# Optimization experiments

Measured on AMD Instinct MI355X. Metric: run time of the kernel, lower is better.

Reference implementation:

```python
import jax, jax.numpy as jnp
import numpy as np

D_MODEL = 1024
D_INNER = 2 * D_MODEL        # mambapy default expand=2
D_STATE = 16                 # mambapy default
D_CONV = 4                   # mambapy default
DT_RANK = D_MODEL // 16      # ceil(1024/16) = 64
D_FF = 4 * D_MODEL
BATCH = 2
SEQ = 2048


def setup_inputs() -> dict:
    key = jax.random.key(0)
    ks = jax.random.split(key, 12)
    s = 0.02
    rn = lambda k, shape: jax.random.normal(k, shape, jnp.float32) * s
    inp = {
        'x': jax.random.normal(ks[0], (BATCH, SEQ, D_MODEL), jnp.float32),
        'ln1_w': jnp.ones((D_MODEL,), jnp.float32),
        'ln1_b': jnp.zeros((D_MODEL,), jnp.float32),
        'in_proj_w': rn(ks[1], (2 * D_INNER, D_MODEL)),
        'conv_w': rn(ks[2], (D_INNER, 1, D_CONV)),
        'conv_b': jnp.zeros((D_INNER,), jnp.float32),
        'x_proj_w': rn(ks[3], (DT_RANK + 2 * D_STATE, D_INNER)),
        'dt_w': rn(ks[4], (D_INNER, DT_RANK)),
        'dt_b': jax.random.normal(ks[5], (D_INNER,), jnp.float32) * 0.5 - 4.0,
        'A_log': jnp.log(jnp.broadcast_to(jnp.arange(1, D_STATE + 1, dtype=jnp.float32), (D_INNER, D_STATE))),
        'Dskip': jnp.ones((D_INNER,), jnp.float32),
        'out_proj_w': rn(ks[6], (D_MODEL, D_INNER)),
        'ln2_w': jnp.ones((D_MODEL,), jnp.float32),
        'ln2_b': jnp.zeros((D_MODEL,), jnp.float32),
        'ff1_w': rn(ks[7], (D_FF, D_MODEL)),
        'ff1_b': jnp.zeros((D_FF,), jnp.float32),
        'ff2_w': rn(ks[8], (D_MODEL, D_FF)),
        'ff2_b': jnp.zeros((D_MODEL,), jnp.float32),
    }
    return inp


def _layernorm(x, w, b, eps=1e-5):
    m = jnp.mean(x, -1, keepdims=True)
    v = jnp.var(x, -1, keepdims=True)
    return (x - m) * jax.lax.rsqrt(v + eps) * w + b


def _mamba(y, in_proj_w, conv_w, conv_b, x_proj_w, dt_w, dt_b, A_log, Dskip, out_proj_w):
    # y: [B, L, d_model]
    xz = y @ in_proj_w.T                       # [B, L, 2*d_inner]
    xc, z = jnp.split(xz, 2, axis=-1)
    # causal depthwise conv1d over seq
    xt = xc.transpose(0, 2, 1)                 # [B, d_inner, L]
    xt = jax.lax.conv_general_dilated(
        xt, conv_w, (1,), [(D_CONV - 1, 0)],
        dimension_numbers=('NCH', 'OIH', 'NCH'),
        feature_group_count=D_INNER) + conv_b[None, :, None]
    u = jax.nn.silu(xt.transpose(0, 2, 1))     # [B, L, d_inner]
    dbc = u @ x_proj_w.T                       # [B, L, dt_rank + 2*d_state]
    dlt = jax.nn.softplus(dbc[..., :DT_RANK] @ dt_w.T + dt_b)   # [B, L, d_inner]
    Bm = dbc[..., DT_RANK:DT_RANK + D_STATE]   # [B, L, d_state]
    Cm = dbc[..., DT_RANK + D_STATE:]          # [B, L, d_state]
    A = -jnp.exp(A_log)                        # [d_inner, d_state]

    def step(h, inp):
        d, Bt, Ct, ut = inp                    # [B,d_inner],[B,d_state],[B,d_state],[B,d_inner]
        h = jnp.exp(d[:, :, None] * A) * h + (d * ut)[:, :, None] * Bt[:, None, :]
        yt = jnp.einsum('bds,bs->bd', h, Ct)
        return h, yt

    h0 = jnp.zeros((y.shape[0], D_INNER, D_STATE), y.dtype)
    xs = (dlt.transpose(1, 0, 2), Bm.transpose(1, 0, 2), Cm.transpose(1, 0, 2), u.transpose(1, 0, 2))
    _, ys = jax.lax.scan(step, h0, xs)         # ys: [L, B, d_inner]
    ysc = ys.transpose(1, 0, 2) + u * Dskip
    return (ysc * jax.nn.silu(z)) @ out_proj_w.T


def reference(x, ln1_w, ln1_b, in_proj_w, conv_w, conv_b, x_proj_w, dt_w, dt_b,
              A_log, Dskip, out_proj_w, ln2_w, ln2_b, ff1_w, ff1_b, ff2_w, ff2_b):
    y = _layernorm(x, ln1_w, ln1_b)
    y = _mamba(y, in_proj_w, conv_w, conv_b, x_proj_w, dt_w, dt_b, A_log, Dskip, out_proj_w)
    y = _layernorm(y, ln2_w, ln2_b)
    h = jax.nn.gelu(y @ ff1_w.T + ff1_b, approximate=False)
    y = h @ ff2_w.T + ff2_b
    return x + y
```

## Files before the change

kernel.cpp:

```cpp
#include <hip/hip_runtime.h>

#define DEV __device__ __forceinline__

typedef float f32x4 __attribute__((ext_vector_type(4)));
typedef short bf16x8 __attribute__((ext_vector_type(8)));

DEV unsigned short f2bf(float f) {
  union { float f; unsigned int u; } v; v.f = f;
  unsigned int r = v.u + 0x7FFFu + ((v.u >> 16) & 1u);
  return (unsigned short)(r >> 16);
}
DEV float bf2f(unsigned short h) {
  union { unsigned int u; float f; } v; v.u = ((unsigned int)h) << 16;
  return v.f;
}

DEV void gload16(const void* g, void* l) {
  __builtin_amdgcn_global_load_lds((const __attribute__((address_space(1))) void*)g,
                                   (__attribute__((address_space(3))) void*)l, 16, 0, 0);
}

template <int EPI>
__global__ __launch_bounds__(256) void gemm_bt(
    const unsigned short* __restrict__ A, const unsigned short* __restrict__ B,
    float* __restrict__ O1, float* __restrict__ O2, unsigned short* __restrict__ Ob,
    const float* __restrict__ bias, const float* __restrict__ resid,
    int M, int N, int K)
{
  __shared__ unsigned short As[128 * 64];
  __shared__ unsigned short Bs[128 * 64];
  const int tid = threadIdx.x;
  const int wave = tid >> 6;
  const int lane = tid & 63;
  const int brow = blockIdx.x * 128;
  const int bcol = blockIdx.y * 128;
  const int wr = (wave >> 1) * 64, wc = (wave & 1) * 64;
  const int lr = lane & 15, lq = lane >> 4;

  f32x4 acc[4][4];
#pragma unroll
  for (int m = 0; m < 4; ++m)
#pragma unroll
    for (int n = 0; n < 4; ++n)
#pragma unroll
      for (int j = 0; j < 4; ++j) acc[m][n][j] = 0.f;

  const size_t strideA = (size_t)K * 2;
  const char* Abase = (const char*)A + (size_t)brow * strideA;
  const char* Bbase = (const char*)B + (size_t)bcol * strideA;

  for (int k0 = 0; k0 < K; k0 += 64) {
#pragma unroll
    for (int is = 0; is < 4; ++is) {
      const int f = is * 4096 + tid * 16;
      const int row = f >> 7, colb = f & 127;
      char* la = (char*)As + is * 4096 + wave * 1024;
      char* lb = (char*)Bs + is * 4096 + wave * 1024;
      gload16(Abase + (size_t)row * strideA + (size_t)k0 * 2 + colb, la);
      gload16(Bbase + (size_t)row * strideA + (size_t)k0 * 2 + colb, lb);
    }
    asm volatile("s_waitcnt vmcnt(0)" ::: "memory");
    __syncthreads();
#pragma unroll
    for (int kk = 0; kk < 2; ++kk) {
      bf16x8 av[4], bv[4];
      const int ko = kk * 32 + lq * 8;
#pragma unroll
      for (int m = 0; m < 4; ++m)
        av[m] = *(const bf16x8*)&As[(wr + m * 16 + lr) * 64 + ko];
#pragma unroll
      for (int n = 0; n < 4; ++n)
        bv[n] = *(const bf16x8*)&Bs[(wc + n * 16 + lr) * 64 + ko];
#pragma unroll
      for (int m = 0; m < 4; ++m)
#pragma unroll
        for (int n = 0; n < 4; ++n)
          acc[m][n] = __builtin_amdgcn_mfma_f32_16x16x32_bf16(av[m], bv[n], acc[m][n], 0, 0, 0);
    }
    __syncthreads();
  }

#pragma unroll
  for (int m = 0; m < 4; ++m) {
#pragma unroll
    for (int n = 0; n < 4; ++n) {
      const int col = bcol + wc + n * 16 + lr;
      const int row0 = brow + wr + m * 16 + lq * 4;
#pragma unroll
      for (int j = 0; j < 4; ++j) {
        const int row = row0 + j;
        float v = acc[m][n][j];
        if (EPI == 0) {
          O1[(size_t)row * N + col] = v;
        } else if (EPI == 1) {
          v += bias[col];
          v = 0.5f * v * (1.f + erff(v * 0.70710678118654752f));
          Ob[(size_t)row * N + col] = f2bf(v);
        } else if (EPI == 2) {
          v += bias[col] + resid[(size_t)row * N + col];
          O1[(size_t)row * N + col] = v;
        } else if (EPI == 3) {
          v += bias[col];
          v = (v > 20.f) ? v : log1pf(expf(v));
          O1[(size_t)row * N + col] = v;
        } else {
          if (col < 2048) O1[(size_t)row * 2048 + col] = v;
          else O2[(size_t)row * 2048 + (col - 2048)] = v / (1.f + expf(-v));
        }
      }
    }
  }
}

__global__ __launch_bounds__(256) void ln_kernel(
    const float* __restrict__ x, const float* __restrict__ w,
    const float* __restrict__ b, unsigned short* __restrict__ out)
{
  const int row = blockIdx.x;
  const int tid = threadIdx.x;
  const float4 v = ((const float4*)(x + (size_t)row * 1024))[tid];
  float s = v.x + v.y + v.z + v.w;
  float sq = v.x * v.x + v.y * v.y + v.z * v.z + v.w * v.w;
#pragma unroll
  for (int m = 32; m >= 1; m >>= 1) { s += __shfl_xor(s, m); sq += __shfl_xor(sq, m); }
  __shared__ float ss[4], sqs[4];
  const int wave = tid >> 6;
  if ((tid & 63) == 0) { ss[wave] = s; sqs[wave] = sq; }
  __syncthreads();
  s = ss[0] + ss[1] + ss[2] + ss[3];
  sq = sqs[0] + sqs[1] + sqs[2] + sqs[3];
  const float mean = s * (1.f / 1024.f);
  const float var = sq * (1.f / 1024.f) - mean * mean;
  const float rstd = rsqrtf(var + 1e-5f);
  const float4 wv = ((const float4*)w)[tid];
  const float4 bv = ((const float4*)b)[tid];
  ushort4 o;
  o.x = f2bf((v.x - mean) * rstd * wv.x + bv.x);
  o.y = f2bf((v.y - mean) * rstd * wv.y + bv.y);
  o.z = f2bf((v.z - mean) * rstd * wv.z + bv.z);
  o.w = f2bf((v.w - mean) * rstd * wv.w + bv.w);
  ((ushort4*)(out + (size_t)row * 1024))[tid] = o;
}

__global__ __launch_bounds__(256) void conv_silu_kernel(
    const float* __restrict__ xc, const float* __restrict__ cw,
    const float* __restrict__ cb, unsigned short* __restrict__ u16)
{
  const int idx = blockIdx.x * 256 + threadIdx.x;
  const int d = idx & 2047;
  const int i = idx >> 11;
  const int t = i & 2047;
  float acc = cb[d];
#pragma unroll
  for (int k = 0; k < 4; ++k) {
    const int tt = t - 3 + k;
    if (tt >= 0) acc += xc[(size_t)(i - 3 + k) * 2048 + d] * cw[d * 4 + k];
  }
  const float s = acc / (1.f + expf(-acc));
  u16[idx] = f2bf(s);
}

__global__ void cvt_bf16_kernel(const float* __restrict__ s, unsigned short* __restrict__ d, int n4) {
  const int i = blockIdx.x * 256 + threadIdx.x;
  if (i >= n4) return;
  const float4 v = ((const float4*)s)[i];
  const ushort4 o = make_ushort4(f2bf(v.x), f2bf(v.y), f2bf(v.z), f2bf(v.w));
  ((ushort4*)d)[i] = o;
}

__global__ void cvt_xprojw_kernel(const float* __restrict__ s, unsigned short* __restrict__ d) {
  const int i = blockIdx.x * 256 + threadIdx.x;
  const int r = (i * 4) >> 11;
  ushort4 o;
  if (r < 96) {
    const float4 v = ((const float4*)s)[i];
    o = make_ushort4(f2bf(v.x), f2bf(v.y), f2bf(v.z), f2bf(v.w));
  } else {
    o = make_ushort4(0, 0, 0, 0);
  }
  ((ushort4*)d)[i] = o;
}

__global__ void cvt_adt_kernel(const float* __restrict__ dbc, unsigned short* __restrict__ adt) {
  const int idx = blockIdx.x * 256 + threadIdx.x;
  const int i = idx >> 6, r = idx & 63;
  adt[idx] = f2bf(dbc[(size_t)i * 128 + r]);
}

template <int NC>
__global__ __launch_bounds__(256) void scan_p1(
    const float* __restrict__ dlt, const unsigned short* __restrict__ u16,
    const float* __restrict__ dbc, const float* __restrict__ A_log,
    float* __restrict__ hpart, float* __restrict__ sdtp)
{
  constexpr int L = 2048 / NC;
  const int tid = threadIdx.x;
  const int c = blockIdx.x % NC;
  const int chg = blockIdx.x / NC;
  const int id = chg * 256 + tid;
  const int dch = id & 2047;
  const int b = id >> 11;
  float al2[16], h[16];
#pragma unroll
  for (int s = 0; s < 16; ++s) {
    al2[s] = -__expf(A_log[dch * 16 + s]) * 1.44269504f;
    h[s] = 0.f;
  }
  const int i0 = b * 2048 + c * L;
  float sdt = 0.f;
  for (int t = 0; t < L; ++t) {
    const size_t i = (size_t)(i0 + t);
    const float dt = dlt[i * 2048 + dch];
    const float uu = bf2f(u16[i * 2048 + dch]);
    const float dtu = dt * uu;
    const float* Bp = dbc + i * 128 + 64;
    const f32x4 B0 = *(const f32x4*)(Bp + 0);
    const f32x4 B1 = *(const f32x4*)(Bp + 4);
    const f32x4 B2 = *(const f32x4*)(Bp + 8);
    const f32x4 B3 = *(const f32x4*)(Bp + 12);
    sdt += dt;
#pragma unroll
    for (int s = 0; s < 16; ++s) {
      const float Bv = (s < 4) ? B0[s & 3] : (s < 8) ? B1[s & 3] : (s < 12) ? B2[s & 3] : B3[s & 3];
      h[s] = exp2f(dt * al2[s]) * h[s] + dtu * Bv;
    }
  }
  float* hp = hpart + ((size_t)(b * NC + c) * 2048 + dch) * 16;
#pragma unroll
  for (int s = 0; s < 16; ++s) hp[s] = h[s];
  sdtp[(size_t)(b * NC + c) * 2048 + dch] = sdt;
}

__global__ __launch_bounds__(256) void scan_prefix(
    const float* __restrict__ hpart, const float* __restrict__ sdtp,
    const float* __restrict__ A_log, float* __restrict__ hpre, int NC)
{
  const int g = blockIdx.x * 256 + threadIdx.x;
  const int s = g & 15;
  const int dch = (g >> 4) & 2047;
  const int b = g >> 15;
  const float al2 = -__expf(A_log[dch * 16 + s]) * 1.44269504f;
  float run = 0.f;
  for (int c = 0; c < NC; ++c) {
    const size_t base = ((size_t)(b * NC + c) * 2048 + dch) * 16 + s;
    hpre[base] = run;
    run = exp2f(al2 * sdtp[(size_t)(b * NC + c) * 2048 + dch]) * run + hpart[base];
  }
}

template <int NC>
__global__ __launch_bounds__(256) void scan_p2(
    const float* __restrict__ dlt, const unsigned short* u16,
    const float* __restrict__ dbc, const float* __restrict__ zs,
    const float* __restrict__ A_log, const float* __restrict__ Dskip,
    const float* __restrict__ hpre, unsigned short* gated)
{
  constexpr int L = 2048 / NC;
  const int tid = threadIdx.x;
  const int c = blockIdx.x % NC;
  const int chg = blockIdx.x / NC;
  const int id = chg * 256 + tid;
  const int dch = id & 2047;
  const int b = id >> 11;
  float al2[16], h[16];
#pragma unroll
  for (int s = 0; s < 16; ++s)
    al2[s] = -__expf(A_log[dch * 16 + s]) * 1.44269504f;
  const float* hb = hpre + ((size_t)(b * NC + c) * 2048 + dch) * 16;
#pragma unroll
  for (int s = 0; s < 16; ++s) h[s] = hb[s];
  const float Dsk = Dskip[dch];
  const int i0 = b * 2048 + c * L;
  for (int t = 0; t < L; ++t) {
    const size_t i = (size_t)(i0 + t);
    const float dt = dlt[i * 2048 + dch];
    const float uu = bf2f(u16[i * 2048 + dch]);
    const float zz = zs[i * 2048 + dch];
    const float dtu = dt * uu;
    const float* Bp = dbc + i * 128 + 64;
    const f32x4 B0 = *(const f32x4*)(Bp + 0);
    const f32x4 B1 = *(const f32x4*)(Bp + 4);
    const f32x4 B2 = *(const f32x4*)(Bp + 8);
    const f32x4 B3 = *(const f32x4*)(Bp + 12);
    const f32x4 C0 = *(const f32x4*)(Bp + 16);
    const f32x4 C1 = *(const f32x4*)(Bp + 20);
    const f32x4 C2 = *(const f32x4*)(Bp + 24);
    const f32x4 C3 = *(const f32x4*)(Bp + 28);
    float y0 = 0.f, y1 = 0.f, y2 = 0.f, y3 = 0.f;
#pragma unroll
    for (int s = 0; s < 16; ++s) {
      const float Bv = (s < 4) ? B0[s & 3] : (s < 8) ? B1[s & 3] : (s < 12) ? B2[s & 3] : B3[s & 3];
      const float Cv = (s < 4) ? C0[s & 3] : (s < 8) ? C1[s & 3] : (s < 12) ? C2[s & 3] : C3[s & 3];
      h[s] = exp2f(dt * al2[s]) * h[s] + dtu * Bv;
      if ((s & 3) == 0) y0 += h[s] * Cv;
      else if ((s & 3) == 1) y1 += h[s] * Cv;
      else if ((s & 3) == 2) y2 += h[s] * Cv;
      else y3 += h[s] * Cv;
    }
    const float y = (y0 + y1) + (y2 + y3);
    gated[i * 2048 + dch] = f2bf((y + uu * Dsk) * zz);
  }
}

extern "C" void kernel_launch(void* const* d_in, const int* in_sizes, int n_in,
                              void* d_out, int out_size, void* d_ws, size_t ws_size,
                              hipStream_t stream) {
  const float* x         = (const float*)d_in[0];
  const float* ln1_w     = (const float*)d_in[1];
  const float* ln1_b     = (const float*)d_in[2];
  const float* in_proj_w = (const float*)d_in[3];
  const float* conv_w    = (const float*)d_in[4];
  const float* conv_b    = (const float*)d_in[5];
  const float* x_proj_w  = (const float*)d_in[6];
  const float* dt_w      = (const float*)d_in[7];
  const float* dt_b      = (const float*)d_in[8];
  const float* A_log     = (const float*)d_in[9];
  const float* Dskip     = (const float*)d_in[10];
  const float* out_proj_w= (const float*)d_in[11];
  const float* ln2_w     = (const float*)d_in[12];
  const float* ln2_b     = (const float*)d_in[13];
  const float* ff1_w     = (const float*)d_in[14];
  const float* ff1_b     = (const float*)d_in[15];
  const float* ff2_w     = (const float*)d_in[16];
  const float* ff2_b     = (const float*)d_in[17];
  float* out = (float*)d_out;

  char* ws = (char*)d_ws;
  size_t off = 0;
  auto alloc = [&](size_t bytes) {
    char* p = ws + off;
    off += (bytes + 255) & ~(size_t)255;
    return p;
  };
  unsigned short* w16_in  = (unsigned short*)alloc(4096ull * 1024 * 2);
  unsigned short* w16_xp  = (unsigned short*)alloc(128ull * 2048 * 2);
  unsigned short* w16_dt  = (unsigned short*)alloc(2048ull * 64 * 2);
  unsigned short* w16_out = (unsigned short*)alloc(1024ull * 2048 * 2);
  unsigned short* w16_ff1 = (unsigned short*)alloc(4096ull * 1024 * 2);
  unsigned short* w16_ff2 = (unsigned short*)alloc(1024ull * 4096 * 2);
  unsigned short* y16     = (unsigned short*)alloc(4096ull * 1024 * 2);
  float* xcbuf            = (float*)alloc(4096ull * 2048 * 4);
  unsigned short* u16     = (unsigned short*)alloc(4096ull * 2048 * 2);
  float* slotA            = (float*)alloc(2048ull * 4096 * 4);
  float* zs               = (float*)alloc(2048ull * 4096 * 4);
  float* dbc              = (float*)alloc(4096ull * 128 * 4);
  unsigned short* adt16   = (unsigned short*)alloc(4096ull * 64 * 2);
  float* dlt              = (float*)alloc(2048ull * 4096 * 4);
  (void)ws_size; (void)in_sizes; (void)n_in; (void)out_size;

  constexpr int NC = 128;
  float* c2 = xcbuf;
  unsigned short* t2_16 = (unsigned short*)((char*)xcbuf + 4096ull * 1024 * 4);
  unsigned short* gated16 = u16;
  float* hpart = slotA;
  unsigned short* h16 = (unsigned short*)slotA;
  float* hpre  = xcbuf;
  float* sdtp  = (float*)y16;

  cvt_bf16_kernel<<<4096, 256, 0, stream>>>(in_proj_w, w16_in, 1048576);
  cvt_xprojw_kernel<<<256, 256, 0, stream>>>(x_proj_w, w16_xp);
  cvt_bf16_kernel<<<128, 256, 0, stream>>>(dt_w, w16_dt, 32768);
  cvt_bf16_kernel<<<2048, 256, 0, stream>>>(out_proj_w, w16_out, 524288);
  cvt_bf16_kernel<<<4096, 256, 0, stream>>>(ff1_w, w16_ff1, 1048576);
  cvt_bf16_kernel<<<4096, 256, 0, stream>>>(ff2_w, w16_ff2, 1048576);

  ln_kernel<<<4096, 256, 0, stream>>>(x, ln1_w, ln1_b, y16);
  gemm_bt<5><<<dim3(32, 32), 256, 0, stream>>>(y16, w16_in, xcbuf, zs, nullptr, nullptr, nullptr, 4096, 4096, 1024);
  conv_silu_kernel<<<32768, 256, 0, stream>>>(xcbuf, conv_w, conv_b, u16);
  gemm_bt<0><<<dim3(32, 1), 256, 0, stream>>>(u16, w16_xp, dbc, nullptr, nullptr, nullptr, nullptr, 4096, 128, 2048);
  cvt_adt_kernel<<<1024, 256, 0, stream>>>(dbc, adt16);
  gemm_bt<3><<<dim3(32, 16), 256, 0, stream>>>(adt16, w16_dt, dlt, nullptr, nullptr, dt_b, nullptr, 4096, 2048, 64);
  scan_p1<NC><<<16 * NC, 256, 0, stream>>>(dlt, u16, dbc, A_log, hpart, sdtp);
  scan_prefix<<<256, 256, 0, stream>>>(hpart, sdtp, A_log, hpre, NC);
  scan_p2<NC><<<16 * NC, 256, 0, stream>>>(dlt, u16, dbc, zs, A_log, Dskip, hpre, gated16);
  gemm_bt<0><<<dim3(32, 8), 256, 0, stream>>>(gated16, w16_out, c2, nullptr, nullptr, nullptr, nullptr, 4096, 1024, 2048);
  ln_kernel<<<4096, 256, 0, stream>>>(c2, ln2_w, ln2_b, t2_16);
  gemm_bt<1><<<dim3(32, 32), 256, 0, stream>>>(t2_16, w16_ff1, nullptr, nullptr, h16, ff1_b, nullptr, 4096, 4096, 1024);
  gemm_bt<2><<<dim3(32, 8), 256, 0, stream>>>(h16, w16_ff2, out, nullptr, nullptr, ff2_b, x, 4096, 1024, 4096);
}
```

Baseline: 720.4 us.

## Merge weight conversion launches, use hardware exp2, and stream pointers in scan

Six separate weight-conversion kernel launches become one combined kernel that dispatches on block index. The scan kernels now use the hardware v_exp_f32 instruction in place of library exp2f and __expf. Their per-step index arithmetic is replaced by incrementing pointers, with a wave-uniform base for the B/C loads, and restrict qualifiers are added. The gated output moves to a different buffer so it no longer aliases u16. The hardware exp trades some precision and denormal handling for fewer instructions in the scan's inner loop.

```diff
diff --git a/kernel.cpp b/kernel.cpp
--- a/kernel.cpp
+++ b/kernel.cpp
@@ -13,6 +13,18 @@
 DEV float bf2f(unsigned short h) {
   union { unsigned int u; float f; } v; v.u = ((unsigned int)h) << 16;
   return v.f;
+}
+
+DEV float fexp2(float x) {
+#if defined(__has_builtin)
+#if __has_builtin(__builtin_amdgcn_exp2f)
+  return __builtin_amdgcn_exp2f(x);
+#else
+  float r; asm("v_exp_f32 %0, %1" : "=v"(r) : "v"(x)); return r;
+#endif
+#else
+  float r; asm("v_exp_f32 %0, %1" : "=v"(r) : "v"(x)); return r;
+#endif
 }
 
 DEV void gload16(const void* g, void* l) {
@@ -160,25 +172,41 @@
   u16[idx] = f2bf(s);
 }
 
-__global__ void cvt_bf16_kernel(const float* __restrict__ s, unsigned short* __restrict__ d, int n4) {
-  const int i = blockIdx.x * 256 + threadIdx.x;
-  if (i >= n4) return;
-  const float4 v = ((const float4*)s)[i];
-  const ushort4 o = make_ushort4(f2bf(v.x), f2bf(v.y), f2bf(v.z), f2bf(v.w));
-  ((ushort4*)d)[i] = o;
-}
-
-__global__ void cvt_xprojw_kernel(const float* __restrict__ s, unsigned short* __restrict__ d) {
-  const int i = blockIdx.x * 256 + threadIdx.x;
-  const int r = (i * 4) >> 11;
-  ushort4 o;
-  if (r < 96) {
+__global__ __launch_bounds__(256) void cvt_weights(
+    const float* __restrict__ w_in, unsigned short* __restrict__ d_in16,
+    const float* __restrict__ w_ff1, unsigned short* __restrict__ d_ff1,
+    const float* __restrict__ w_ff2, unsigned short* __restrict__ d_ff2,
+    const float* __restrict__ w_out, unsigned short* __restrict__ d_out16,
+    const float* __restrict__ w_dt, unsigned short* __restrict__ d_dt,
+    const float* __restrict__ w_xp, unsigned short* __restrict__ d_xp)
+{
+  const int bid = blockIdx.x;
+  const int tid = threadIdx.x;
+  if (bid < 14336) {
+    const float* s; unsigned short* d; int lb;
+    if (bid < 4096)       { s = w_in;  d = d_in16;  lb = bid; }
+    else if (bid < 8192)  { s = w_ff1; d = d_ff1;   lb = bid - 4096; }
+    else if (bid < 12288) { s = w_ff2; d = d_ff2;   lb = bid - 8192; }
+    else if (bid < 14336) { s = w_out; d = d_out16; lb = bid - 12288; }
+    const int i = lb * 256 + tid;
     const float4 v = ((const float4*)s)[i];
-    o = make_ushort4(f2bf(v.x), f2bf(v.y), f2bf(v.z), f2bf(v.w));
+    ((ushort4*)d)[i] = make_ushort4(f2bf(v.x), f2bf(v.y), f2bf(v.z), f2bf(v.w));
+  } else if (bid < 14464) {
+    const int i = (bid - 14336) * 256 + tid;
+    const float4 v = ((const float4*)w_dt)[i];
+    ((ushort4*)d_dt)[i] = make_ushort4(f2bf(v.x), f2bf(v.y), f2bf(v.z), f2bf(v.w));
   } else {
-    o = make_ushort4(0, 0, 0, 0);
-  }
-  ((ushort4*)d)[i] = o;
+    const int i = (bid - 14464) * 256 + tid;
+    const int r = (i * 4) >> 11;
+    ushort4 o;
+    if (r < 96) {
+      const float4 v = ((const float4*)w_xp)[i];
+      o = make_ushort4(f2bf(v.x), f2bf(v.y), f2bf(v.z), f2bf(v.w));
+    } else {
+      o = make_ushort4(0, 0, 0, 0);
+    }
+    ((ushort4*)d_xp)[i] = o;
+  }
 }
 
 __global__ void cvt_adt_kernel(const float* __restrict__ dbc, unsigned short* __restrict__ adt) {
@@ -203,27 +231,30 @@
   float al2[16], h[16];
 #pragma unroll
   for (int s = 0; s < 16; ++s) {
-    al2[s] = -__expf(A_log[dch * 16 + s]) * 1.44269504f;
+    al2[s] = -fexp2(A_log[dch * 16 + s] * 1.44269504f) * 1.44269504f;
     h[s] = 0.f;
   }
   const int i0 = b * 2048 + c * L;
+  const int i0u = __builtin_amdgcn_readfirstlane(i0);
+  const float* dptr = dlt + (size_t)i0 * 2048 + dch;
+  const unsigned short* uptr = u16 + (size_t)i0 * 2048 + dch;
+  const float* Bptr = dbc + (size_t)i0u * 128 + 64;
   float sdt = 0.f;
   for (int t = 0; t < L; ++t) {
-    const size_t i = (size_t)(i0 + t);
-    const float dt = dlt[i * 2048 + dch];
-    const float uu = bf2f(u16[i * 2048 + dch]);
+    const float dt = *dptr;
+    const float uu = bf2f(*uptr);
     const float dtu = dt * uu;
-    const float* Bp = dbc + i * 128 + 64;
-    const f32x4 B0 = *(const f32x4*)(Bp + 0);
-    const f32x4 B1 = *(const f32x4*)(Bp + 4);
-    const f32x4 B2 = *(const f32x4*)(Bp + 8);
-    const f32x4 B3 = *(const f32x4*)(Bp + 12);
+    const f32x4 B0 = *(const f32x4*)(Bptr + 0);
+    const f32x4 B1 = *(const f32x4*)(Bptr + 4);
+    const f32x4 B2 = *(const f32x4*)(Bptr + 8);
+    const f32x4 B3 = *(const f32x4*)(Bptr + 12);
     sdt += dt;
 #pragma unroll
     for (int s = 0; s < 16; ++s) {
       const float Bv = (s < 4) ? B0[s & 3] : (s < 8) ? B1[s & 3] : (s < 12) ? B2[s & 3] : B3[s & 3];
-      h[s] = exp2f(dt * al2[s]) * h[s] + dtu * Bv;
-    }
+      h[s] = fexp2(dt * al2[s]) * h[s] + dtu * Bv;
+    }
+    dptr += 2048; uptr += 2048; Bptr += 128;
   }
   float* hp = hpart + ((size_t)(b * NC + c) * 2048 + dch) * 16;
 #pragma unroll
@@ -239,21 +270,21 @@
   const int s = g & 15;
   const int dch = (g >> 4) & 2047;
   const int b = g >> 15;
-  const float al2 = -__expf(A_log[dch * 16 + s]) * 1.44269504f;
+  const float al2 = -fexp2(A_log[dch * 16 + s] * 1.44269504f) * 1.44269504f;
   float run = 0.f;
   for (int c = 0; c < NC; ++c) {
     const size_t base = ((size_t)(b * NC + c) * 2048 + dch) * 16 + s;
     hpre[base] = run;
-    run = exp2f(al2 * sdtp[(size_t)(b * NC + c) * 2048 + dch]) * run + hpart[base];
+    run = fexp2(al2 * sdtp[(size_t)(b * NC + c) * 2048 + dch]) * run + hpart[base];
   }
 }
 
 template <int NC>
 __global__ __launch_bounds__(256) void scan_p2(
-    const float* __restrict__ dlt, const unsigned short* u16,
+    const float* __restrict__ dlt, const unsigned short* __restrict__ u16,
     const float* __restrict__ dbc, const float* __restrict__ zs,
     const float* __restrict__ A_log, const float* __restrict__ Dskip,
-    const float* __restrict__ hpre, unsigned short* gated)
+    const float* __restrict__ hpre, unsigned short* __restrict__ gated)
 {
   constexpr int L = 2048 / NC;
   const int tid = threadIdx.x;
@@ -265,40 +296,45 @@
   float al2[16], h[16];
 #pragma unroll
   for (int s = 0; s < 16; ++s)
-    al2[s] = -__expf(A_log[dch * 16 + s]) * 1.44269504f;
+    al2[s] = -fexp2(A_log[dch * 16 + s] * 1.44269504f) * 1.44269504f;
   const float* hb = hpre + ((size_t)(b * NC + c) * 2048 + dch) * 16;
 #pragma unroll
   for (int s = 0; s < 16; ++s) h[s] = hb[s];
   const float Dsk = Dskip[dch];
   const int i0 = b * 2048 + c * L;
+  const int i0u = __builtin_amdgcn_readfirstlane(i0);
+  const float* dptr = dlt + (size_t)i0 * 2048 + dch;
+  const unsigned short* uptr = u16 + (size_t)i0 * 2048 + dch;
+  const float* zptr = zs + (size_t)i0 * 2048 + dch;
+  const float* Bptr = dbc + (size_t)i0u * 128 + 64;
+  unsigned short* gptr = gated + (size_t)i0 * 2048 + dch;
   for (int t = 0; t < L; ++t) {
-    const size_t i = (size_t)(i0 + t);
-    const float dt = dlt[i * 2048 + dch];
-    const float uu = bf2f(u16[i * 2048 + dch]);
-    const float zz = zs[i * 2048 + dch];
+    const float dt = *dptr;
+    const float uu = bf2f(*uptr);
+    const float zz = *zptr;
     const float dtu = dt * uu;
-    const float* Bp = dbc + i * 128 + 64;
-    const f32x4 B0 = *(const f32x4*)(Bp + 0);
-    const f32x4 B1 = *(const f32x4*)(Bp + 4);
-    const f32x4 B2 = *(const f32x4*)(Bp + 8);
-    const f32x4 B3 = *(const f32x4*)(Bp + 12);
-    const f32x4 C0 = *(const f32x4*)(Bp + 16);
-    const f32x4 C1 = *(const f32x4*)(Bp + 20);
-    const f32x4 C2 = *(const f32x4*)(Bp + 24);
-    const f32x4 C3 = *(const f32x4*)(Bp + 28);
+    const f32x4 B0 = *(const f32x4*)(Bptr + 0);
+    const f32x4 B1 = *(const f32x4*)(Bptr + 4);
+    const f32x4 B2 = *(const f32x4*)(Bptr + 8);
+    const f32x4 B3 = *(const f32x4*)(Bptr + 12);
+    const f32x4 C0 = *(const f32x4*)(Bptr + 16);
+    const f32x4 C1 = *(const f32x4*)(Bptr + 20);
+    const f32x4 C2 = *(const f32x4*)(Bptr + 24);
+    const f32x4 C3 = *(const f32x4*)(Bptr + 28);
     float y0 = 0.f, y1 = 0.f, y2 = 0.f, y3 = 0.f;
 #pragma unroll
     for (int s = 0; s < 16; ++s) {
       const float Bv = (s < 4) ? B0[s & 3] : (s < 8) ? B1[s & 3] : (s < 12) ? B2[s & 3] : B3[s & 3];
       const float Cv = (s < 4) ? C0[s & 3] : (s < 8) ? C1[s & 3] : (s < 12) ? C2[s & 3] : C3[s & 3];
-      h[s] = exp2f(dt * al2[s]) * h[s] + dtu * Bv;
+      h[s] = fexp2(dt * al2[s]) * h[s] + dtu * Bv;
       if ((s & 3) == 0) y0 += h[s] * Cv;
       else if ((s & 3) == 1) y1 += h[s] * Cv;
       else if ((s & 3) == 2) y2 += h[s] * Cv;
       else y3 += h[s] * Cv;
     }
     const float y = (y0 + y1) + (y2 + y3);
-    gated[i * 2048 + dch] = f2bf((y + uu * Dsk) * zz);
+    *gptr = f2bf((y + uu * Dsk) * zz);
+    dptr += 2048; uptr += 2048; zptr += 2048; Bptr += 128; gptr += 2048;
   }
 }
 
@@ -351,18 +387,15 @@
   constexpr int NC = 128;
   float* c2 = xcbuf;
   unsigned short* t2_16 = (unsigned short*)((char*)xcbuf + 4096ull * 1024 * 4);
-  unsigned short* gated16 = u16;
   float* hpart = slotA;
+  unsigned short* gated16 = (unsigned short*)slotA;
   unsigned short* h16 = (unsigned short*)slotA;
   float* hpre  = xcbuf;
   float* sdtp  = (float*)y16;
 
-  cvt_bf16_kernel<<<4096, 256, 0, stream>>>(in_proj_w, w16_in, 1048576);
-  cvt_xprojw_kernel<<<256, 256, 0, stream>>>(x_proj_w, w16_xp);
-  cvt_bf16_kernel<<<128, 256, 0, stream>>>(dt_w, w16_dt, 32768);
-  cvt_bf16_kernel<<<2048, 256, 0, stream>>>(out_proj_w, w16_out, 524288);
-  cvt_bf16_kernel<<<4096, 256, 0, stream>>>(ff1_w, w16_ff1, 1048576);
-  cvt_bf16_kernel<<<4096, 256, 0, stream>>>(ff2_w, w16_ff2, 1048576);
+  cvt_weights<<<14720, 256, 0, stream>>>(in_proj_w, w16_in, ff1_w, w16_ff1,
+                                         ff2_w, w16_ff2, out_proj_w, w16_out,
+                                         dt_w, w16_dt, x_proj_w, w16_xp);
 
   ln_kernel<<<4096, 256, 0, stream>>>(x, ln1_w, ln1_b, y16);
   gemm_bt<5><<<dim3(32, 32), 256, 0, stream>>>(y16, w16_in, xcbuf, zs, nullptr, nullptr, nullptr, 4096, 4096, 1024);
```

After: 626.6 us. 13.0% less time.
